# Kernel optimization log

Hardware: AMD Instinct MI355X
Metric: run time of the kernel (lower is better)

The kernel has to match this reference:

```python
import jax, jax.numpy as jnp
import numpy as np

LEAKY_SLOPE = 0.2
EPS = 1e-9


def setup_inputs() -> dict:
    key = jax.random.key(0)
    k1, k2, k3, k4 = jax.random.split(key, 4)
    B, N, F_in, F_out = 4, 4096, 128, 64
    h = jax.random.normal(k1, (B, N, F_in), dtype=jnp.float32)
    adj = jax.random.uniform(k2, (B, N, N), dtype=jnp.float32)
    W = jax.random.normal(k3, (F_in, F_out), dtype=jnp.float32) * (1.0 / np.sqrt(F_in))
    a = jax.random.normal(k4, (2 * F_out, 1), dtype=jnp.float32) * (1.0 / np.sqrt(2 * F_out))
    return {"h": h, "adj": adj, "W": W, "a": a}


def reference(h, adj, W, a):
    # h: [B,N,F_in], adj: [B,N,N], W: [F_in,F_out], a: [2F_out,1]
    Wh = jnp.einsum('bnf,fo->bno', h, W)  # [B,N,F_out]
    F_out = W.shape[1]
    a1 = a[:F_out, 0]   # applied to Wh1 (neighbor j features)
    a2 = a[F_out:, 0]   # applied to Wh2 (center i features)
    s1 = Wh @ a1        # [B,N] -> broadcast over j axis
    s2 = Wh @ a2        # [B,N] -> broadcast over i axis
    # e[b,i,j] = leaky_relu(Wh[b,j]@a1 + Wh[b,i]@a2)  (concat([Wh1,Wh2]) @ a)
    e = jax.nn.leaky_relu(s2[:, :, None] + s1[:, None, :], negative_slope=LEAKY_SLOPE)
    attn = jax.nn.softmax(e, axis=-1)          # dense softmax over all nodes
    attn = attn * adj                          # mask with adjacency
    attn = attn / (jnp.sum(attn, axis=-1, keepdims=True) + EPS)  # renormalize
    return jnp.einsum('bij,bjo->bio', attn, Wh)  # [B,N,F_out]
```

## Files before the change

### kernel.cpp

```cpp
#include <hip/hip_runtime.h>
#include <hip/hip_bf16.h>


typedef __attribute__((ext_vector_type(8))) short bf16x8;
typedef __attribute__((ext_vector_type(4))) float f32x4;
typedef __attribute__((ext_vector_type(4))) unsigned int u32x4;

#define LOG2E 1.4426950408889634f

__device__ __forceinline__ unsigned int pk2(float lo, float hi) {
  float2 f2; f2.x = lo; f2.y = hi;
  union { __hip_bfloat162 b; unsigned int u; } c;
  c.b = __float22bfloat162_rn(f2);
  return c.u;
}
__device__ __forceinline__ bf16x8 u2b(u32x4 v) {
  union { u32x4 u; bf16x8 b; } c; c.u = v; return c.b;
}
__device__ __forceinline__ float vexp2_(float x) {
  float r; asm("v_exp_f32 %0, %1" : "=v"(r) : "v"(x)); return r;
}

__global__ __launch_bounds__(256) void k_wh(
    const float* __restrict__ h, const float* __restrict__ W, const float* __restrict__ a,
    unsigned short* __restrict__ wt, float* __restrict__ s1, float* __restrict__ s2) {
  __shared__ float hs[32][130];
  __shared__ float Ws[128 * 64];
  const int t = threadIdx.x;
  const int b = blockIdx.x >> 7;
  const int row0 = (blockIdx.x & 127) << 5;

  #pragma unroll
  for (int it = 0; it < 8; ++it) {
    const int fidx = it * 256 + t;
    ((float4*)Ws)[fidx] = ((const float4*)W)[fidx];
  }
  #pragma unroll
  for (int it = 0; it < 4; ++it) {
    int flat = it * 256 + t;
    int r = flat >> 5, q = flat & 31;
    const float4 v = *(const float4*)(h + ((size_t)(b * 4096 + row0 + r)) * 128 + 4 * q);
    hs[r][4*q+0] = v.x; hs[r][4*q+1] = v.y; hs[r][4*q+2] = v.z; hs[r][4*q+3] = v.w;
  }
  __syncthreads();

  const int rg = t >> 4, cg = t & 15;
  float acc[2][4] = {};
  for (int k = 0; k < 128; ++k) {
    float4 wv = ((const float4*)Ws)[k * 16 + cg];
    #pragma unroll
    for (int i = 0; i < 2; ++i) {
      float hv = hs[2*rg + i][k];
      acc[i][0] = fmaf(hv, wv.x, acc[i][0]);
      acc[i][1] = fmaf(hv, wv.y, acc[i][1]);
      acc[i][2] = fmaf(hv, wv.z, acc[i][2]);
      acc[i][3] = fmaf(hv, wv.w, acc[i][3]);
    }
  }
  __syncthreads();

  float (*WhF)[68] = (float(*)[68])hs;
  #pragma unroll
  for (int i = 0; i < 2; ++i)
    #pragma unroll
    for (int j = 0; j < 4; ++j)
      WhF[2*rg + i][4*cg + j] = acc[i][j];
  __syncthreads();

  if (t < 32) {
    float x1 = 0.f, x2 = 0.f;
    #pragma unroll 8
    for (int c = 0; c < 64; ++c) {
      float v = WhF[t][c];
      x1 = fmaf(v, a[c], x1);
      x2 = fmaf(v, a[64 + c], x2);
    }
    s1[b * 4096 + row0 + t] = x1 * LOG2E;
    s2[b * 4096 + row0 + t] = x2 * LOG2E;
  }

  const int col = t >> 2, sub = t & 3;
  unsigned int uh[4];
  #pragma unroll
  for (int r = 0; r < 4; ++r)
    uh[r] = pk2(WhF[8*sub + 2*r][col], WhF[8*sub + 2*r + 1][col]);
  const int S = (b * 128 + (row0 >> 5)) * 4 + (col >> 4);
  unsigned short* dst = wt + ((size_t)S << 9) + sub * 128 + (col & 15) * 8;
  *(uint4*)dst = make_uint4(uh[0], uh[1], uh[2], uh[3]);
}

__global__ __launch_bounds__(256, 4) void k_main(
    const float* __restrict__ adj, const unsigned short* __restrict__ wt,
    const float* __restrict__ s1, const float* __restrict__ s2,
    float* __restrict__ out) {
  __shared__ unsigned short Pws[2][2048];
  __shared__ float Ss[16];

  const int t = threadIdx.x;
  const int blk = blockIdx.x;
  const int xcd = blk & 7;
  const int b = xcd >> 1;
  const int tile = (blk >> 3) + ((xcd & 1) << 7);
  const int row0 = tile << 4;
  const int l = t & 63, w = t >> 6;
  const int lr = l & 15, g = l >> 4;
  const int lh = l >> 5, lc = l & 31;

  const float* adjW = adj + ((size_t)(b * 4096 + row0 + 4 * w + lh)) * 4096 + 4 * lc;
  const float* s1W  = s1 + b * 4096 + 4 * lc;
  const unsigned short* wtW = wt + (((size_t)b * 512 + w) << 9) + 8 * l;

  float s2v[2];
  #pragma unroll
  for (int i = 0; i < 2; ++i)
    s2v[i] = s2[b * 4096 + row0 + 4 * w + 2 * i + lh];

  float sar[2] = {0.f, 0.f};
  f32x4 acc = {0.f, 0.f, 0.f, 0.f};

  f32x4 aX[2], aY[2], sX, sY;
  u32x4 bv[4];

#define LOADADJ(av, sv, ks) do {                                              \
    const int ko = ((ks) & 31) << 7;                                          \
    av[0] = *(const f32x4*)(adjW + ko);                                       \
    av[1] = *(const f32x4*)(adjW + 8192 + ko);                                \
    sv = *(const f32x4*)(s1W + ko);                                           \
  } while (0)

#define LOADB(ks) do {                                                        \
    const int ksm = (ks) & 31;                                                \
    _Pragma("unroll")                                                         \
    for (int kk = 0; kk < 4; ++kk)                                            \
      bv[kk] = *(const u32x4*)(wtW + (size_t)(ksm * 4 + kk) * 2048);          \
  } while (0)

#define PBUILD(av, sv, buf) do {                                              \
    unsigned short* Pd = &Pws[buf][0];                                        \
    _Pragma("unroll")                                                         \
    for (int i = 0; i < 2; ++i) {                                             \
      const int rl = 4 * w + 2 * i + lh;                                      \
      float e0 = s2v[i] + sv[0], e1 = s2v[i] + sv[1];                         \
      float e2 = s2v[i] + sv[2], e3 = s2v[i] + sv[3];                         \
      e0 = fmaxf(e0, 0.2f * e0); e1 = fmaxf(e1, 0.2f * e1);                   \
      e2 = fmaxf(e2, 0.2f * e2); e3 = fmaxf(e3, 0.2f * e3);                   \
      float p0 = vexp2_(e0), p1 = vexp2_(e1);                                 \
      float p2 = vexp2_(e2), p3 = vexp2_(e3);                                 \
      float w0 = av[i][0] * p0, w1 = av[i][1] * p1;                           \
      float w2 = av[i][2] * p2, w3 = av[i][3] * p3;                           \
      sar[i] += (w0 + w1) + (w2 + w3);                                        \
      uint2 pk; pk.x = pk2(w0, w1); pk.y = pk2(w2, w3);                       \
      *(uint2*)(Pd + rl * 128 + ((4 * lc) ^ ((rl & 7) << 3))) = pk;           \
    }                                                                         \
  } while (0)

#define SYNC() do {                                                           \
    asm volatile("s_waitcnt lgkmcnt(0)" ::: "memory");                        \
    __builtin_amdgcn_sched_barrier(0);                                        \
    __builtin_amdgcn_s_barrier();                                             \
    __builtin_amdgcn_sched_barrier(0);                                        \
  } while (0)

#define MFMAP(buf) do {                                                       \
    const unsigned short* Pr = &Pws[buf][0];                                  \
    _Pragma("unroll")                                                         \
    for (int kk = 0; kk < 4; ++kk) {                                          \
      const int koff = (8 * g + 32 * kk) ^ ((lr & 7) << 3);                   \
      bf16x8 a0 = *(const bf16x8*)(Pr + lr * 128 + koff);                     \
      acc = __builtin_amdgcn_mfma_f32_16x16x32_bf16(a0, u2b(bv[kk]), acc, 0, 0, 0); \
    }                                                                         \
  } while (0)

  LOADADJ(aX, sX, 0);
  LOADADJ(aY, sY, 1);
  LOADB(0);

  for (int it = 0; it < 16; ++it) {
    PBUILD(aX, sX, 0);
    LOADADJ(aX, sX, 2 * it + 2);
    SYNC();
    MFMAP(0);
    LOADB(2 * it + 1);

    PBUILD(aY, sY, 1);
    LOADADJ(aY, sY, 2 * it + 3);
    SYNC();
    MFMAP(1);
    LOADB(2 * it + 2);
  }

  #pragma unroll
  for (int i = 0; i < 2; ++i) {
    float v = sar[i];
    #pragma unroll
    for (int m = 1; m < 32; m <<= 1) v += __shfl_xor(v, m);
    if (lc == 0) Ss[4 * w + 2 * i + lh] = v;
  }
  __syncthreads();

  #pragma unroll
  for (int reg = 0; reg < 4; ++reg) {
    const int r = 4 * g + reg;
    const float inv = 1.0f / Ss[r];
    out[((size_t)(b * 4096 + row0 + r)) * 64 + 16 * w + lr] = acc[reg] * inv;
  }
}

extern "C" void kernel_launch(void* const* d_in, const int* in_sizes, int n_in,
                              void* d_out, int out_size, void* d_ws, size_t ws_size,
                              hipStream_t stream) {
  const float* h   = (const float*)d_in[0];
  const float* adj = (const float*)d_in[1];
  const float* W   = (const float*)d_in[2];
  const float* a   = (const float*)d_in[3];
  float* out = (float*)d_out;

  unsigned short* wt = (unsigned short*)d_ws;
  float* s1 = (float*)(wt + (size_t)4 * 64 * 4096);
  float* s2 = s1 + 16384;

  k_wh  <<<512, 256, 0, stream>>>(h, W, a, wt, s1, s2);
  k_main<<<1024, 256, 0, stream>>>(adj, wt, s1, s2, out);
}
```

Measured before the change: 66.82 us.

## Give each wave a full 16-row tile and build MFMA A-fragments in registers

Each wave now owns an independent 16-row output tile across all 64 output columns. It computes the exp-weighted adjacency values straight into MFMA A-operand registers, so the LDS staging buffer and per-step block barriers are gone. The grid shrinks from 1024 to 256 blocks, and the row-sum reduction becomes wave-local shuffles. The trade-off is higher register pressure (double-buffered adj, s1 and B fragments) and fewer blocks. Each wave also reloads the full Wh B-operand, which raises L2 traffic for wt compared with sharing it across waves.

```diff
diff --git a/kernel.cpp b/kernel.cpp
--- a/kernel.cpp
+++ b/kernel.cpp
@@ -89,120 +89,96 @@
   *(uint4*)dst = make_uint4(uh[0], uh[1], uh[2], uh[3]);
 }
 
-__global__ __launch_bounds__(256, 4) void k_main(
+__global__ __launch_bounds__(256) void k_main(
     const float* __restrict__ adj, const unsigned short* __restrict__ wt,
     const float* __restrict__ s1, const float* __restrict__ s2,
     float* __restrict__ out) {
-  __shared__ unsigned short Pws[2][2048];
-  __shared__ float Ss[16];
-
   const int t = threadIdx.x;
+  const int l = t & 63, w = t >> 6;
   const int blk = blockIdx.x;
   const int xcd = blk & 7;
   const int b = xcd >> 1;
-  const int tile = (blk >> 3) + ((xcd & 1) << 7);
+  const int tile = ((blk >> 3) + ((xcd & 1) << 5)) * 4 + w;
   const int row0 = tile << 4;
-  const int l = t & 63, w = t >> 6;
   const int lr = l & 15, g = l >> 4;
-  const int lh = l >> 5, lc = l & 31;
-
-  const float* adjW = adj + ((size_t)(b * 4096 + row0 + 4 * w + lh)) * 4096 + 4 * lc;
-  const float* s1W  = s1 + b * 4096 + 4 * lc;
-  const unsigned short* wtW = wt + (((size_t)b * 512 + w) << 9) + 8 * l;
-
-  float s2v[2];
-  #pragma unroll
-  for (int i = 0; i < 2; ++i)
-    s2v[i] = s2[b * 4096 + row0 + 4 * w + 2 * i + lh];
-
-  float sar[2] = {0.f, 0.f};
-  f32x4 acc = {0.f, 0.f, 0.f, 0.f};
-
-  f32x4 aX[2], aY[2], sX, sY;
-  u32x4 bv[4];
+
+  const float* adjW = adj + ((size_t)(b * 4096 + row0 + lr)) * 4096 + 8 * g;
+  const float* s1W  = s1 + b * 4096 + 8 * g;
+  const float s2v   = s2[b * 4096 + row0 + lr];
+  const unsigned short* wtW = wt + ((size_t)b << 18) + 8 * l;
+
+  float sar = 0.f;
+  f32x4 acc[4] = {{0.f,0.f,0.f,0.f},{0.f,0.f,0.f,0.f},{0.f,0.f,0.f,0.f},{0.f,0.f,0.f,0.f}};
+
+  f32x4 aX[2][2], aY[2][2], sXv[2][2], sYv[2][2];
+  u32x4 bvX[8], bvY[8];
 
 #define LOADADJ(av, sv, ks) do {                                              \
-    const int ko = ((ks) & 31) << 7;                                          \
-    av[0] = *(const f32x4*)(adjW + ko);                                       \
-    av[1] = *(const f32x4*)(adjW + 8192 + ko);                                \
-    sv = *(const f32x4*)(s1W + ko);                                           \
-  } while (0)
-
-#define LOADB(ks) do {                                                        \
-    const int ksm = (ks) & 31;                                                \
+    const int ko = ((ks) & 63) << 6;                                          \
     _Pragma("unroll")                                                         \
-    for (int kk = 0; kk < 4; ++kk)                                            \
-      bv[kk] = *(const u32x4*)(wtW + (size_t)(ksm * 4 + kk) * 2048);          \
-  } while (0)
-
-#define PBUILD(av, sv, buf) do {                                              \
-    unsigned short* Pd = &Pws[buf][0];                                        \
-    _Pragma("unroll")                                                         \
-    for (int i = 0; i < 2; ++i) {                                             \
-      const int rl = 4 * w + 2 * i + lh;                                      \
-      float e0 = s2v[i] + sv[0], e1 = s2v[i] + sv[1];                         \
-      float e2 = s2v[i] + sv[2], e3 = s2v[i] + sv[3];                         \
-      e0 = fmaxf(e0, 0.2f * e0); e1 = fmaxf(e1, 0.2f * e1);                   \
-      e2 = fmaxf(e2, 0.2f * e2); e3 = fmaxf(e3, 0.2f * e3);                   \
-      float p0 = vexp2_(e0), p1 = vexp2_(e1);                                 \
-      float p2 = vexp2_(e2), p3 = vexp2_(e3);                                 \
-      float w0 = av[i][0] * p0, w1 = av[i][1] * p1;                           \
-      float w2 = av[i][2] * p2, w3 = av[i][3] * p3;                           \
-      sar[i] += (w0 + w1) + (w2 + w3);                                        \
-      uint2 pk; pk.x = pk2(w0, w1); pk.y = pk2(w2, w3);                       \
-      *(uint2*)(Pd + rl * 128 + ((4 * lc) ^ ((rl & 7) << 3))) = pk;           \
+    for (int kk = 0; kk < 2; ++kk) {                                          \
+      av[kk][0] = *(const f32x4*)(adjW + ko + 32 * kk);                       \
+      av[kk][1] = *(const f32x4*)(adjW + ko + 32 * kk + 4);                   \
+      sv[kk][0] = *(const f32x4*)(s1W + ko + 32 * kk);                        \
+      sv[kk][1] = *(const f32x4*)(s1W + ko + 32 * kk + 4);                    \
     }                                                                         \
   } while (0)
 
-#define SYNC() do {                                                           \
-    asm volatile("s_waitcnt lgkmcnt(0)" ::: "memory");                        \
-    __builtin_amdgcn_sched_barrier(0);                                        \
-    __builtin_amdgcn_s_barrier();                                             \
-    __builtin_amdgcn_sched_barrier(0);                                        \
+#define LOADB(bv, ks) do {                                                    \
+    const int k32 = ((ks) & 63) << 1;                                         \
+    _Pragma("unroll")                                                         \
+    for (int kk = 0; kk < 2; ++kk)                                            \
+      _Pragma("unroll")                                                       \
+      for (int cg = 0; cg < 4; ++cg)                                          \
+        bv[kk*4+cg] = *(const u32x4*)(wtW + ((size_t)((k32+kk)*4+cg) << 9));  \
   } while (0)
 
-#define MFMAP(buf) do {                                                       \
-    const unsigned short* Pr = &Pws[buf][0];                                  \
+#define STEPX(av, sv, bv) do {                                                \
     _Pragma("unroll")                                                         \
-    for (int kk = 0; kk < 4; ++kk) {                                          \
-      const int koff = (8 * g + 32 * kk) ^ ((lr & 7) << 3);                   \
-      bf16x8 a0 = *(const bf16x8*)(Pr + lr * 128 + koff);                     \
-      acc = __builtin_amdgcn_mfma_f32_16x16x32_bf16(a0, u2b(bv[kk]), acc, 0, 0, 0); \
+    for (int kk = 0; kk < 2; ++kk) {                                          \
+      float wv[8];                                                            \
+      _Pragma("unroll")                                                       \
+      for (int j = 0; j < 8; ++j) {                                           \
+        float e = s2v + sv[kk][j >> 2][j & 3];                                \
+        e = fmaxf(e, 0.2f * e);                                               \
+        float p = vexp2_(e);                                                  \
+        wv[j] = av[kk][j >> 2][j & 3] * p;                                    \
+        sar += wv[j];                                                         \
+      }                                                                       \
+      union { unsigned int s[4]; u32x4 v; } fu;                               \
+      fu.s[0] = pk2(wv[0], wv[1]); fu.s[1] = pk2(wv[2], wv[3]);               \
+      fu.s[2] = pk2(wv[4], wv[5]); fu.s[3] = pk2(wv[6], wv[7]);               \
+      const bf16x8 frA = u2b(fu.v);                                           \
+      _Pragma("unroll")                                                       \
+      for (int cg = 0; cg < 4; ++cg)                                          \
+        acc[cg] = __builtin_amdgcn_mfma_f32_16x16x32_bf16(                    \
+            frA, u2b(bv[kk*4+cg]), acc[cg], 0, 0, 0);                         \
     }                                                                         \
   } while (0)
 
-  LOADADJ(aX, sX, 0);
-  LOADADJ(aY, sY, 1);
-  LOADB(0);
-
-  for (int it = 0; it < 16; ++it) {
-    PBUILD(aX, sX, 0);
-    LOADADJ(aX, sX, 2 * it + 2);
-    SYNC();
-    MFMAP(0);
-    LOADB(2 * it + 1);
-
-    PBUILD(aY, sY, 1);
-    LOADADJ(aY, sY, 2 * it + 3);
-    SYNC();
-    MFMAP(1);
-    LOADB(2 * it + 2);
-  }
-
-  #pragma unroll
-  for (int i = 0; i < 2; ++i) {
-    float v = sar[i];
+  LOADADJ(aX, sXv, 0); LOADB(bvX, 0);
+  LOADADJ(aY, sYv, 1); LOADB(bvY, 1);
+
+  for (int it = 0; it < 32; ++it) {
+    STEPX(aX, sXv, bvX);
+    LOADADJ(aX, sXv, 2 * it + 2);
+    LOADB(bvX, 2 * it + 2);
+    STEPX(aY, sYv, bvY);
+    LOADADJ(aY, sYv, 2 * it + 3);
+    LOADB(bvY, 2 * it + 3);
+  }
+
+  sar += __shfl_xor(sar, 16);
+  sar += __shfl_xor(sar, 32);
+  const float inv = 1.0f / sar;
+
+  #pragma unroll
+  for (int reg = 0; reg < 4; ++reg) {
+    const float invr = __shfl(inv, 4 * g + reg);
+    const size_t ob = ((size_t)(b * 4096 + row0 + 4 * g + reg)) * 64 + lr;
     #pragma unroll
-    for (int m = 1; m < 32; m <<= 1) v += __shfl_xor(v, m);
-    if (lc == 0) Ss[4 * w + 2 * i + lh] = v;
-  }
-  __syncthreads();
-
-  #pragma unroll
-  for (int reg = 0; reg < 4; ++reg) {
-    const int r = 4 * g + reg;
-    const float inv = 1.0f / Ss[r];
-    out[((size_t)(b * 4096 + row0 + r)) * 64 + 16 * w + lr] = acc[reg] * inv;
+    for (int cg = 0; cg < 4; ++cg)
+      out[ob + 16 * cg] = acc[cg][reg] * invr;
   }
 }
 
@@ -220,5 +196,5 @@
   float* s2 = s1 + 16384;
 
   k_wh  <<<512, 256, 0, stream>>>(h, W, a, wt, s1, s2);
-  k_main<<<1024, 256, 0, stream>>>(adj, wt, s1, s2, out);
-}
+  k_main<<<256, 256, 0, stream>>>(adj, wt, s1, s2, out);
+}
```

Result: slower. 81.77 us (+22.4%).
